# Kernel optimization log

Hardware: AMD Instinct MI355X
Metric: run time of the kernel (lower is better)

## Reference

```python
import jax, jax.numpy as jnp
import numpy as np

M = 100000   # rows of sparse matrix B
K = 100000   # cols of sparse matrix B / rows of dense A
N = 64       # cols of dense A
NNZ = 1600000

def setup_inputs() -> dict:
    key = jax.random.key(0)
    k1, k2, k3, k4 = jax.random.split(key, 4)
    vals = jax.random.normal(k1, (NNZ,), dtype=jnp.float32)
    A = jax.random.normal(k2, (K, N), dtype=jnp.float32)
    rows = jax.random.randint(k3, (NNZ,), 0, M, dtype=jnp.int32)
    cols = jax.random.randint(k4, (NNZ,), 0, K, dtype=jnp.int32)
    return {"vals": vals, "A": A, "rows": rows, "cols": cols}

def reference(vals, A, rows, cols):
    # out[m, n] = sum_{k in nnz(row m)} B[m,k] * A[k,n]
    contrib = A[cols] * vals[:, None]            # [NNZ, N] gather + scale
    out = jax.ops.segment_sum(contrib, rows, num_segments=M)  # scatter-add -> [M, N]
    return out
```

## Files before the change

kernel.cpp:

```cpp
#include <hip/hip_runtime.h>
#include <hip/hip_bf16.h>


#define NCOLS      64
#define RPB        64
#define RPB_SHIFT  6
#define NBLK       256
#define BT         256
#define CAP_S      8192
#define CAP_R      2048
#define SCAP       12
#define MAXNB      1568

__global__ void spmm_scatter_atomic(const float* __restrict__ vals,
                                    const float* __restrict__ A,
                                    const int* __restrict__ rows,
                                    const int* __restrict__ cols,
                                    float* __restrict__ out,
                                    int nnz) {
    int t = blockIdx.x * blockDim.x + threadIdx.x;
    int e = t >> 4;
    int q = t & 15;
    if (e >= nnz) return;
    float v = vals[e];
    int   r = rows[e];
    int   c = cols[e];
    const float4 a = *reinterpret_cast<const float4*>(A + (size_t)c * NCOLS + q * 4);
    float* o = out + (size_t)r * NCOLS + q * 4;
    atomicAdd(o + 0, v * a.x);
    atomicAdd(o + 1, v * a.y);
    atomicAdd(o + 2, v * a.z);
    atomicAdd(o + 3, v * a.w);
}

__global__ void conv_a_bf16(const float* __restrict__ A, uint* __restrict__ Abf,
                            int n) {
    int i = blockIdx.x * blockDim.x + threadIdx.x;
    int idx = i << 3;
    if (idx >= n) return;
    const uint4 u0 = *reinterpret_cast<const uint4*>(A + idx);
    const uint4 u1 = *reinterpret_cast<const uint4*>(A + idx + 4);
    auto bf = [](uint u) -> uint { return (u + 0x7FFFu + ((u >> 16) & 1u)) >> 16; };
    uint4 o;
    o.x = bf(u0.x) | (bf(u0.y) << 16);
    o.y = bf(u0.z) | (bf(u0.w) << 16);
    o.z = bf(u1.x) | (bf(u1.y) << 16);
    o.w = bf(u1.z) | (bf(u1.w) << 16);
    *reinterpret_cast<uint4*>(Abf + (i << 2)) = o;
}

__global__ void __launch_bounds__(BT)
sort_scatter(const float* __restrict__ vals,
             const int* __restrict__ rows,
             const int* __restrict__ cols,
             int2* __restrict__ pvc,
             int* __restrict__ tab,
             int nnz, int chunk, int NB) {
    __shared__ int2 sorted[CAP_S];
    __shared__ int  cnt[MAXNB];
    __shared__ int  sc[BT];

    int j = blockIdx.x, t = threadIdx.x;
    int base = j * chunk;
    int n = nnz - base;
    if (n > chunk) n = chunk;
    if (n < 0) n = 0;

    for (int i = t; i < NB; i += BT) cnt[i] = 0;
    __syncthreads();
    for (int i = t; i < n; i += BT)
        atomicAdd(&cnt[rows[base + i] >> RPB_SHIFT], 1);
    __syncthreads();

    int spt = (NB + BT - 1) / BT;
    int lo = t * spt, hi = min(lo + spt, NB);
    int s = 0;
    for (int i = lo; i < hi; ++i) s += cnt[i];
    sc[t] = s;
    __syncthreads();
    for (int off = 1; off < BT; off <<= 1) {
        int u = (t >= off) ? sc[t - off] : 0;
        __syncthreads();
        sc[t] += u;
        __syncthreads();
    }
    int run = sc[t] - s;
    for (int i = lo; i < hi; ++i) { int c = cnt[i]; cnt[i] = run; run += c; }
    __syncthreads();

    for (int b = t; b < NB; b += BT) tab[(size_t)j * (NB + 1) + b] = base + cnt[b];
    if (t == 0) tab[(size_t)j * (NB + 1) + NB] = base + n;
    __syncthreads();

    for (int i = t; i < n; i += BT) {
        int e = base + i;
        int r = rows[e];
        int slot = atomicAdd(&cnt[r >> RPB_SHIFT], 1);
        sorted[slot] = make_int2(__float_as_int(vals[e]),
                                 cols[e] | ((r & (RPB - 1)) << 17));
    }
    __syncthreads();

    for (int i = t; i < n; i += BT) pvc[base + i] = sorted[i];
}

template<int USEBF>
__global__ void __launch_bounds__(BT)
spmm_reduce_rs(const int2* __restrict__ pvc,
               const int* __restrict__ tab,
               const float* __restrict__ A,
               const uint* __restrict__ Abf,
               float* __restrict__ out,
               int M, int NB) {
    __shared__ int2 sorted[CAP_R];
    __shared__ int  cnt[RPB];
    __shared__ int  off[RPB + 1];
    __shared__ int  red[BT];

    int b = blockIdx.x, t = threadIdx.x;
    int sS = tab[(size_t)t * (NB + 1) + b];
    int sE = tab[(size_t)t * (NB + 1) + b + 1];
    int len = sE - sS;

    if (t < RPB) cnt[t] = 0;
    red[t] = len;
    __syncthreads();
    for (int o = BT / 2; o > 0; o >>= 1) {
        if (t < o) red[t] += red[t + o];
        __syncthreads();
    }
    int total = red[0];
    int row0 = b << RPB_SHIFT;
    int nrow = min(RPB, M - row0);

    if (total > CAP_R) {
        for (int i = t; i < nrow * NCOLS; i += BT) out[(size_t)row0 * NCOLS + i] = 0.f;
        __syncthreads();
        for (int e = sS; e < sE; ++e) {
            int2 vc = pvc[e];
            float v = __int_as_float(vc.x);
            int   c = vc.y & 0x1FFFF;
            int   rl = (vc.y >> 17) & (RPB - 1);
            for (int nn = 0; nn < NCOLS; ++nn)
                atomicAdd(&out[(size_t)(row0 + rl) * NCOLS + nn],
                          v * A[(size_t)c * NCOLS + nn]);
        }
        return;
    }

    int2 st[SCAP];
    #pragma unroll
    for (int i = 0; i < SCAP; ++i) {
        if (i < len) {
            st[i] = pvc[sS + i];
            atomicAdd(&cnt[(st[i].y >> 17) & (RPB - 1)], 1);
        }
    }
    for (int i = SCAP; i < len; ++i)
        atomicAdd(&cnt[(pvc[sS + i].y >> 17) & (RPB - 1)], 1);
    __syncthreads();

    if (t < RPB) {
        int v = cnt[t];
        int s = v;
        #pragma unroll
        for (int d = 1; d < RPB; d <<= 1) {
            int u = __shfl_up(s, d, 64);
            if (t >= d) s += u;
        }
        off[t + 1] = s;
        if (t == 0) off[0] = 0;
        cnt[t] = s - v;
    }
    __syncthreads();

    #pragma unroll
    for (int i = 0; i < SCAP; ++i) {
        if (i < len) {
            int slot = atomicAdd(&cnt[(st[i].y >> 17) & (RPB - 1)], 1);
            sorted[slot] = st[i];
        }
    }
    for (int i = SCAP; i < len; ++i) {
        int2 vc = pvc[sS + i];
        int slot = atomicAdd(&cnt[(vc.y >> 17) & (RPB - 1)], 1);
        sorted[slot] = vc;
    }
    __syncthreads();

    int lane = t & 7;
    int grp  = t >> 3;
    float acc0[8], acc1[8];
    #pragma unroll
    for (int i = 0; i < 8; ++i) { acc0[i] = 0.f; acc1[i] = 0.f; }

    #pragma unroll
    for (int r = 0; r < 2; ++r) {
        float* acc = r ? acc1 : acc0;
        int lr = (grp << 1) + r;
        int s0 = off[lr], s1 = off[lr + 1];
        for (int e = s0; e < s1; ++e) {
            int2 vc = sorted[e];
            float v = __int_as_float(vc.x);
            int   c = vc.y & 0x1FFFF;
            if (USEBF) {
                const uint4 u = *reinterpret_cast<const uint4*>(
                    Abf + ((size_t)c << 5) + (lane << 2));
                acc[0] += v * __uint_as_float(u.x << 16);
                acc[1] += v * __uint_as_float(u.x & 0xFFFF0000u);
                acc[2] += v * __uint_as_float(u.y << 16);
                acc[3] += v * __uint_as_float(u.y & 0xFFFF0000u);
                acc[4] += v * __uint_as_float(u.z << 16);
                acc[5] += v * __uint_as_float(u.z & 0xFFFF0000u);
                acc[6] += v * __uint_as_float(u.w << 16);
                acc[7] += v * __uint_as_float(u.w & 0xFFFF0000u);
            } else {
                const float4 a0 = *reinterpret_cast<const float4*>(
                    A + ((size_t)c << 6) + (lane << 3));
                const float4 a1 = *reinterpret_cast<const float4*>(
                    A + ((size_t)c << 6) + (lane << 3) + 4);
                acc[0] += v * a0.x; acc[1] += v * a0.y;
                acc[2] += v * a0.z; acc[3] += v * a0.w;
                acc[4] += v * a1.x; acc[5] += v * a1.y;
                acc[6] += v * a1.z; acc[7] += v * a1.w;
            }
        }
    }

    int m0 = row0 + (grp << 1);
    if (m0 < M) {
        float4* o = reinterpret_cast<float4*>(out + (size_t)m0 * NCOLS + (lane << 3));
        o[0] = make_float4(acc0[0], acc0[1], acc0[2], acc0[3]);
        o[1] = make_float4(acc0[4], acc0[5], acc0[6], acc0[7]);
    }
    if (m0 + 1 < M) {
        float4* o = reinterpret_cast<float4*>(out + (size_t)(m0 + 1) * NCOLS + (lane << 3));
        o[0] = make_float4(acc1[0], acc1[1], acc1[2], acc1[3]);
        o[1] = make_float4(acc1[4], acc1[5], acc1[6], acc1[7]);
    }
}

extern "C" void kernel_launch(void* const* d_in, const int* in_sizes, int n_in,
                              void* d_out, int out_size, void* d_ws, size_t ws_size,
                              hipStream_t stream) {
    const float* vals = (const float*)d_in[0];
    const float* A    = (const float*)d_in[1];
    const int*   rows = (const int*)d_in[2];
    const int*   cols = (const int*)d_in[3];
    float*       out  = (float*)d_out;

    const int nnz = in_sizes[0];
    const int na  = in_sizes[1];
    const int M   = out_size / NCOLS;
    const int K   = na / NCOLS;

    const int NB    = (M + RPB - 1) >> RPB_SHIFT;
    const int chunk = (nnz + NBLK - 1) / NBLK;

    size_t off_tab = 0;
    size_t tab_sz  = (size_t)NBLK * (NB + 1) * 4;
    size_t off_pvc = (off_tab + tab_sz + 15) & ~(size_t)15;
    size_t off_abf = (off_pvc + (size_t)nnz * 8 + 15) & ~(size_t)15;
    size_t need_f32 = off_pvc + (size_t)nnz * 8;
    size_t need_bf  = off_abf + (size_t)na * 2;

    if (need_f32 > ws_size || chunk > CAP_S || NB > MAXNB ||
        K > (1 << 17) || (na & 7) != 0) {
        hipMemsetAsync(d_out, 0, (size_t)out_size * sizeof(float), stream);
        int threads_total = nnz * 16;
        int block = 256;
        int grid = (threads_total + block - 1) / block;
        spmm_scatter_atomic<<<grid, block, 0, stream>>>(vals, A, rows, cols, out, nnz);
        return;
    }

    char* ws = (char*)d_ws;
    int*  tab = (int*)(ws + off_tab);
    int2* pvc = (int2*)(ws + off_pvc);
    uint* abf = (uint*)(ws + off_abf);

    const bool use_bf = (need_bf <= ws_size);

    if (use_bf) {
        int nthr = na / 8;
        conv_a_bf16<<<(nthr + 255) / 256, 256, 0, stream>>>(A, abf, na);
    }
    sort_scatter<<<NBLK, BT, 0, stream>>>(vals, rows, cols, pvc, tab, nnz, chunk, NB);
    if (use_bf)
        spmm_reduce_rs<1><<<NB, BT, 0, stream>>>(pvc, tab, A, abf, out, M, NB);
    else
        spmm_reduce_rs<0><<<NB, BT, 0, stream>>>(pvc, tab, A, abf, out, M, NB);
}
```

Measured before the change: 91.31 us.

## Vectorize sort loads/stores, drop block reduction, and widen per-thread row work

The sort kernel now reads rows, vals and cols as 4-wide vectors and writes the bucketed pairs back as 16-byte stores. The chunk size is rounded up to a multiple of 4 so each block's base stays aligned for those loads. The reduce kernel drops the shared-memory tree reduction and takes the block total from the per-row prefix sum, which it now computes before the overflow check. Each row is now handled by 4 threads with 16 accumulators instead of 8 threads each covering two rows, which issues wider A gathers but halves the threads per row and raises register use.

New measurement: 78.34 us. 1.17x faster.

```diff
diff --git a/kernel.cpp b/kernel.cpp
--- a/kernel.cpp
+++ b/kernel.cpp
@@ -65,10 +65,20 @@
     int n = nnz - base;
     if (n > chunk) n = chunk;
     if (n < 0) n = 0;
+    int nv = n >> 2;
 
     for (int i = t; i < NB; i += BT) cnt[i] = 0;
     __syncthreads();
-    for (int i = t; i < n; i += BT)
+
+    const int4* r4p = reinterpret_cast<const int4*>(rows + base);
+    for (int i = t; i < nv; i += BT) {
+        int4 r = r4p[i];
+        atomicAdd(&cnt[r.x >> RPB_SHIFT], 1);
+        atomicAdd(&cnt[r.y >> RPB_SHIFT], 1);
+        atomicAdd(&cnt[r.z >> RPB_SHIFT], 1);
+        atomicAdd(&cnt[r.w >> RPB_SHIFT], 1);
+    }
+    for (int i = (nv << 2) + t; i < n; i += BT)
         atomicAdd(&cnt[rows[base + i] >> RPB_SHIFT], 1);
     __syncthreads();
 
@@ -92,7 +102,21 @@
     if (t == 0) tab[(size_t)j * (NB + 1) + NB] = base + n;
     __syncthreads();
 
-    for (int i = t; i < n; i += BT) {
+    const float4* v4p = reinterpret_cast<const float4*>(vals + base);
+    const int4*   c4p = reinterpret_cast<const int4*>(cols + base);
+    for (int i = t; i < nv; i += BT) {
+        int4 r = r4p[i]; float4 v = v4p[i]; int4 c = c4p[i];
+        int slot;
+        slot = atomicAdd(&cnt[r.x >> RPB_SHIFT], 1);
+        sorted[slot] = make_int2(__float_as_int(v.x), c.x | ((r.x & (RPB - 1)) << 17));
+        slot = atomicAdd(&cnt[r.y >> RPB_SHIFT], 1);
+        sorted[slot] = make_int2(__float_as_int(v.y), c.y | ((r.y & (RPB - 1)) << 17));
+        slot = atomicAdd(&cnt[r.z >> RPB_SHIFT], 1);
+        sorted[slot] = make_int2(__float_as_int(v.z), c.z | ((r.z & (RPB - 1)) << 17));
+        slot = atomicAdd(&cnt[r.w >> RPB_SHIFT], 1);
+        sorted[slot] = make_int2(__float_as_int(v.w), c.w | ((r.w & (RPB - 1)) << 17));
+    }
+    for (int i = (nv << 2) + t; i < n; i += BT) {
         int e = base + i;
         int r = rows[e];
         int slot = atomicAdd(&cnt[r >> RPB_SHIFT], 1);
@@ -101,7 +125,13 @@
     }
     __syncthreads();
 
-    for (int i = t; i < n; i += BT) pvc[base + i] = sorted[i];
+    int4* pvc4 = reinterpret_cast<int4*>(pvc + base);
+    int nh = n >> 1;
+    for (int i = t; i < nh; i += BT) {
+        int2 a = sorted[2 * i], b2 = sorted[2 * i + 1];
+        pvc4[i] = make_int4(a.x, a.y, b2.x, b2.y);
+    }
+    if ((n & 1) && t == 0) pvc[base + n - 1] = sorted[n - 1];
 }
 
 template<int USEBF>
@@ -115,7 +145,6 @@
     __shared__ int2 sorted[CAP_R];
     __shared__ int  cnt[RPB];
     __shared__ int  off[RPB + 1];
-    __shared__ int  red[BT];
 
     int b = blockIdx.x, t = threadIdx.x;
     int sS = tab[(size_t)t * (NB + 1) + b];
@@ -123,13 +152,35 @@
     int len = sE - sS;
 
     if (t < RPB) cnt[t] = 0;
-    red[t] = len;
-    __syncthreads();
-    for (int o = BT / 2; o > 0; o >>= 1) {
-        if (t < o) red[t] += red[t + o];
-        __syncthreads();
-    }
-    int total = red[0];
+    __syncthreads();
+
+    int2 st[SCAP];
+    #pragma unroll
+    for (int i = 0; i < SCAP; ++i) {
+        if (i < len) {
+            st[i] = pvc[sS + i];
+            atomicAdd(&cnt[(st[i].y >> 17) & (RPB - 1)], 1);
+        }
+    }
+    for (int i = SCAP; i < len; ++i)
+        atomicAdd(&cnt[(pvc[sS + i].y >> 17) & (RPB - 1)], 1);
+    __syncthreads();
+
+    if (t < RPB) {
+        int v = cnt[t];
+        int s = v;
+        #pragma unroll
+        for (int d = 1; d < RPB; d <<= 1) {
+            int u = __shfl_up(s, d, 64);
+            if (t >= d) s += u;
+        }
+        off[t + 1] = s;
+        if (t == 0) off[0] = 0;
+        cnt[t] = s - v;
+    }
+    __syncthreads();
+
+    int total = off[RPB];
     int row0 = b << RPB_SHIFT;
     int nrow = min(RPB, M - row0);
 
@@ -148,32 +199,6 @@
         return;
     }
 
-    int2 st[SCAP];
-    #pragma unroll
-    for (int i = 0; i < SCAP; ++i) {
-        if (i < len) {
-            st[i] = pvc[sS + i];
-            atomicAdd(&cnt[(st[i].y >> 17) & (RPB - 1)], 1);
-        }
-    }
-    for (int i = SCAP; i < len; ++i)
-        atomicAdd(&cnt[(pvc[sS + i].y >> 17) & (RPB - 1)], 1);
-    __syncthreads();
-
-    if (t < RPB) {
-        int v = cnt[t];
-        int s = v;
-        #pragma unroll
-        for (int d = 1; d < RPB; d <<= 1) {
-            int u = __shfl_up(s, d, 64);
-            if (t >= d) s += u;
-        }
-        off[t + 1] = s;
-        if (t == 0) off[0] = 0;
-        cnt[t] = s - v;
-    }
-    __syncthreads();
-
     #pragma unroll
     for (int i = 0; i < SCAP; ++i) {
         if (i < len) {
@@ -188,55 +213,59 @@
     }
     __syncthreads();
 
-    int lane = t & 7;
-    int grp  = t >> 3;
-    float acc0[8], acc1[8];
+    int lane = t & 3;
+    int grp  = t >> 2;
+    float acc[16];
     #pragma unroll
-    for (int i = 0; i < 8; ++i) { acc0[i] = 0.f; acc1[i] = 0.f; }
-
-    #pragma unroll
-    for (int r = 0; r < 2; ++r) {
-        float* acc = r ? acc1 : acc0;
-        int lr = (grp << 1) + r;
-        int s0 = off[lr], s1 = off[lr + 1];
-        for (int e = s0; e < s1; ++e) {
-            int2 vc = sorted[e];
-            float v = __int_as_float(vc.x);
-            int   c = vc.y & 0x1FFFF;
-            if (USEBF) {
-                const uint4 u = *reinterpret_cast<const uint4*>(
-                    Abf + ((size_t)c << 5) + (lane << 2));
-                acc[0] += v * __uint_as_float(u.x << 16);
-                acc[1] += v * __uint_as_float(u.x & 0xFFFF0000u);
-                acc[2] += v * __uint_as_float(u.y << 16);
-                acc[3] += v * __uint_as_float(u.y & 0xFFFF0000u);
-                acc[4] += v * __uint_as_float(u.z << 16);
-                acc[5] += v * __uint_as_float(u.z & 0xFFFF0000u);
-                acc[6] += v * __uint_as_float(u.w << 16);
-                acc[7] += v * __uint_as_float(u.w & 0xFFFF0000u);
-            } else {
-                const float4 a0 = *reinterpret_cast<const float4*>(
-                    A + ((size_t)c << 6) + (lane << 3));
-                const float4 a1 = *reinterpret_cast<const float4*>(
-                    A + ((size_t)c << 6) + (lane << 3) + 4);
-                acc[0] += v * a0.x; acc[1] += v * a0.y;
-                acc[2] += v * a0.z; acc[3] += v * a0.w;
-                acc[4] += v * a1.x; acc[5] += v * a1.y;
-                acc[6] += v * a1.z; acc[7] += v * a1.w;
-            }
-        }
-    }
-
-    int m0 = row0 + (grp << 1);
-    if (m0 < M) {
-        float4* o = reinterpret_cast<float4*>(out + (size_t)m0 * NCOLS + (lane << 3));
-        o[0] = make_float4(acc0[0], acc0[1], acc0[2], acc0[3]);
-        o[1] = make_float4(acc0[4], acc0[5], acc0[6], acc0[7]);
-    }
-    if (m0 + 1 < M) {
-        float4* o = reinterpret_cast<float4*>(out + (size_t)(m0 + 1) * NCOLS + (lane << 3));
-        o[0] = make_float4(acc1[0], acc1[1], acc1[2], acc1[3]);
-        o[1] = make_float4(acc1[4], acc1[5], acc1[6], acc1[7]);
+    for (int i = 0; i < 16; ++i) acc[i] = 0.f;
+
+    int s0 = off[grp], s1 = off[grp + 1];
+    for (int e = s0; e < s1; ++e) {
+        int2 vc = sorted[e];
+        float v = __int_as_float(vc.x);
+        int   c = vc.y & 0x1FFFF;
+        if (USEBF) {
+            const uint4* p = reinterpret_cast<const uint4*>(
+                Abf + ((size_t)c << 5) + (lane << 3));
+            uint4 u0 = p[0], u1 = p[1];
+            acc[0]  += v * __uint_as_float(u0.x << 16);
+            acc[1]  += v * __uint_as_float(u0.x & 0xFFFF0000u);
+            acc[2]  += v * __uint_as_float(u0.y << 16);
+            acc[3]  += v * __uint_as_float(u0.y & 0xFFFF0000u);
+            acc[4]  += v * __uint_as_float(u0.z << 16);
+            acc[5]  += v * __uint_as_float(u0.z & 0xFFFF0000u);
+            acc[6]  += v * __uint_as_float(u0.w << 16);
+            acc[7]  += v * __uint_as_float(u0.w & 0xFFFF0000u);
+            acc[8]  += v * __uint_as_float(u1.x << 16);
+            acc[9]  += v * __uint_as_float(u1.x & 0xFFFF0000u);
+            acc[10] += v * __uint_as_float(u1.y << 16);
+            acc[11] += v * __uint_as_float(u1.y & 0xFFFF0000u);
+            acc[12] += v * __uint_as_float(u1.z << 16);
+            acc[13] += v * __uint_as_float(u1.z & 0xFFFF0000u);
+            acc[14] += v * __uint_as_float(u1.w << 16);
+            acc[15] += v * __uint_as_float(u1.w & 0xFFFF0000u);
+        } else {
+            const float4* p = reinterpret_cast<const float4*>(
+                A + ((size_t)c << 6) + (lane << 4));
+            float4 a0 = p[0], a1 = p[1], a2 = p[2], a3 = p[3];
+            acc[0]  += v * a0.x; acc[1]  += v * a0.y;
+            acc[2]  += v * a0.z; acc[3]  += v * a0.w;
+            acc[4]  += v * a1.x; acc[5]  += v * a1.y;
+            acc[6]  += v * a1.z; acc[7]  += v * a1.w;
+            acc[8]  += v * a2.x; acc[9]  += v * a2.y;
+            acc[10] += v * a2.z; acc[11] += v * a2.w;
+            acc[12] += v * a3.x; acc[13] += v * a3.y;
+            acc[14] += v * a3.z; acc[15] += v * a3.w;
+        }
+    }
+
+    int m = row0 + grp;
+    if (m < M) {
+        float4* o = reinterpret_cast<float4*>(out + (size_t)m * NCOLS + (lane << 4));
+        o[0] = make_float4(acc[0],  acc[1],  acc[2],  acc[3]);
+        o[1] = make_float4(acc[4],  acc[5],  acc[6],  acc[7]);
+        o[2] = make_float4(acc[8],  acc[9],  acc[10], acc[11]);
+        o[3] = make_float4(acc[12], acc[13], acc[14], acc[15]);
     }
 }
 
@@ -255,7 +284,7 @@
     const int K   = na / NCOLS;
 
     const int NB    = (M + RPB - 1) >> RPB_SHIFT;
-    const int chunk = (nnz + NBLK - 1) / NBLK;
+    const int chunk = (((nnz + NBLK - 1) / NBLK) + 3) & ~3;
 
     size_t off_tab = 0;
     size_t tab_sz  = (size_t)NBLK * (NB + 1) * 4;
```
